# Optimization experiments

Measured on AMD Instinct MI355X. Metric: run time of the kernel, lower is better.

The kernel has to match this reference:

```python
import jax, jax.numpy as jnp
import numpy as np

D_MODEL = 512
N_HEADS = 8
HEAD_DIM = D_MODEL // N_HEADS
BATCH = 4
SEQ = 2048


def setup_inputs() -> dict:
    key = jax.random.key(0)
    ks = jax.random.split(key, 9)
    s = 1.0 / np.sqrt(D_MODEL)
    inp = {
        "x": jax.random.normal(ks[0], (BATCH, SEQ, D_MODEL), dtype=jnp.float32),
        "wq": jax.random.uniform(ks[1], (D_MODEL, D_MODEL), jnp.float32, -s, s),
        "bq": jax.random.uniform(ks[2], (D_MODEL,), jnp.float32, -s, s),
        "wk": jax.random.uniform(ks[3], (D_MODEL, D_MODEL), jnp.float32, -s, s),
        "bk": jax.random.uniform(ks[4], (D_MODEL,), jnp.float32, -s, s),
        "wv": jax.random.uniform(ks[5], (D_MODEL, D_MODEL), jnp.float32, -s, s),
        "bv": jax.random.uniform(ks[6], (D_MODEL,), jnp.float32, -s, s),
        "wo": jax.random.uniform(ks[7], (D_MODEL, D_MODEL), jnp.float32, -s, s),
        "bo": jax.random.uniform(ks[8], (D_MODEL,), jnp.float32, -s, s),
    }
    return inp


def reference(x, wq, bq, wk, bk, wv, bv, wo, bo):
    B, S, D = x.shape
    H, Hd = N_HEADS, HEAD_DIM
    # projections (torch Linear: y = x @ W^T + b; here weights stored as [in, out])
    q = (x @ wq + bq).reshape(B, S, H, Hd).transpose(0, 2, 1, 3)  # [B,H,S,Hd]
    k = (x @ wk + bk).reshape(B, S, H, Hd).transpose(0, 2, 1, 3)
    v = (x @ wv + bv).reshape(B, S, H, Hd).transpose(0, 2, 1, 3)
    scores = jnp.einsum("bhqd,bhkd->bhqk", q, k) / jnp.sqrt(jnp.float32(Hd))
    attn = jax.nn.softmax(scores, axis=-1)
    o = jnp.einsum("bhqk,bhkd->bhqd", attn, v)  # [B,H,S,Hd]
    o = o.transpose(0, 2, 1, 3).reshape(B, S, D)
    return o @ wo + bo
```

## Files before the change

kernel.cpp:

```cpp
#include <hip/hip_runtime.h>
#include <math.h>

#define DM   512
#define SEQL 2048
#define NB   4
#define NH   8
#define HD   64

typedef _Float16 f16;
typedef __fp16   fp16x2 __attribute__((ext_vector_type(2)));
typedef _Float16 f16x4 __attribute__((ext_vector_type(4)));
typedef _Float16 f16x8 __attribute__((ext_vector_type(8)));
typedef float    f32x4 __attribute__((ext_vector_type(4)));

#define QSCALE 0.1803368801f
#define SOFTMAX_SHIFT 4.328085123f
#define PSTR 88

typedef const __attribute__((address_space(1))) void* gp1_t;
typedef __attribute__((address_space(3))) void* lp3_t;
__device__ __forceinline__ void glds16(const void* g, void* l) {
    __builtin_amdgcn_global_load_lds((gp1_t)g, (lp3_t)l, 16, 0, 0);
}

__device__ __forceinline__ float fast_exp2(float x) {
    return __builtin_amdgcn_exp2f(x);
}

__global__ __launch_bounds__(256) void prep_kernel(
    const float* __restrict__ x, f16* __restrict__ xh,
    const float* __restrict__ w0, const float* __restrict__ w1,
    const float* __restrict__ w2, const float* __restrict__ w3,
    f16* __restrict__ o0, f16* __restrict__ o1,
    f16* __restrict__ o2, f16* __restrict__ o3)
{
    __shared__ f16 t[64][72];
    const int bx = blockIdx.x;
    if (bx < 2048) {
        int i = (bx * 256 + threadIdx.x) * 8;
        float4 a = *(const float4*)&x[i];
        float4 b = *(const float4*)&x[i + 4];
        f16x8 h;
        h[0] = (f16)a.x; h[1] = (f16)a.y; h[2] = (f16)a.z; h[3] = (f16)a.w;
        h[4] = (f16)b.x; h[5] = (f16)b.y; h[6] = (f16)b.z; h[7] = (f16)b.w;
        *(f16x8*)&xh[i] = h;
        return;
    }
    const int idx  = bx - 2048;
    const int wsel = idx >> 6, tile = idx & 63;
    const float* w; f16* o;
    switch (wsel) {
        case 0:  w = w0; o = o0; break;
        case 1:  w = w1; o = o1; break;
        case 2:  w = w2; o = o2; break;
        default: w = w3; o = o3; break;
    }
    const int n0 = (tile & 7) * 64, k0 = (tile >> 3) * 64;
    const int tx = threadIdx.x & 63, tg = threadIdx.x >> 6;
    #pragma unroll
    for (int r = 0; r < 16; ++r) {
        int kl = tg * 16 + r;
        t[tx][kl] = (f16)w[(size_t)(k0 + kl) * DM + n0 + tx];
    }
    __syncthreads();
    #pragma unroll
    for (int r = 0; r < 16; ++r) {
        int nl = tg * 16 + r;
        o[(size_t)(n0 + nl) * DM + k0 + tx] = t[nl][tx];
    }
}

__global__ __launch_bounds__(256) void gemm_qkv(
    const f16* __restrict__ A, const f16* __restrict__ Wt,
    const float* __restrict__ bq, const float* __restrict__ bk,
    const float* __restrict__ bv,
    f16* __restrict__ qh, f16* __restrict__ kh, f16* __restrict__ vth)
{
    __shared__ f16 As[2][128 * 32];
    __shared__ f16 Bs[2][128 * 32];

    const int tid  = threadIdx.x;
    const int lane = tid & 63, wave = tid >> 6;
    const int quad = lane >> 4, l15 = lane & 15;
    const int wm = wave >> 1, wn = wave & 1;

    const int bid = blockIdx.x;
    const int r8  = bid & 7;
    const int tt  = bid >> 3;
    const int j   = tt % 12;
    const int mm  = tt / 12;
    const int n0  = j * 128;
    const int m0  = (mm * 8 + r8) * 128;
    const bool qk = (j < 8);

    const int sr16 = lane >> 2;
    const int sk   = (lane & 3) * 8;

    f32x4 acc[4][4] = {};

    for (int k0 = 0; k0 < DM; k0 += 64) {
        #pragma unroll
        for (int kh2 = 0; kh2 < 2; ++kh2) {
            #pragma unroll
            for (int rb = 0; rb < 2; ++rb) {
                const int row = wave * 32 + rb * 16;
                glds16(&A [(size_t)(m0 + row + sr16) * DM + k0 + kh2 * 32 + sk],
                       &As[kh2][row * 32]);
                glds16(&Wt[(size_t)(n0 + row + sr16) * DM + k0 + kh2 * 32 + sk],
                       &Bs[kh2][row * 32]);
            }
        }
        __syncthreads();

        #pragma unroll
        for (int kh2 = 0; kh2 < 2; ++kh2) {
            f16x8 af[4], bf[4];
            #pragma unroll
            for (int i = 0; i < 4; ++i)
                af[i] = *(f16x8*)&As[kh2][(wm * 64 + i * 16 + l15) * 32 + quad * 8];
            #pragma unroll
            for (int i = 0; i < 4; ++i)
                bf[i] = *(f16x8*)&Bs[kh2][(wn * 64 + i * 16 + l15) * 32 + quad * 8];
            if (qk) {
                #pragma unroll
                for (int i = 0; i < 4; ++i)
                    #pragma unroll
                    for (int jj = 0; jj < 4; ++jj)
                        acc[i][jj] = __builtin_amdgcn_mfma_f32_16x16x32_f16(
                            bf[i], af[jj], acc[i][jj], 0, 0, 0);
            } else {
                #pragma unroll
                for (int i = 0; i < 4; ++i)
                    #pragma unroll
                    for (int jj = 0; jj < 4; ++jj)
                        acc[i][jj] = __builtin_amdgcn_mfma_f32_16x16x32_f16(
                            af[i], bf[jj], acc[i][jj], 0, 0, 0);
            }
        }
        __syncthreads();
    }

    const int nwave = n0 + wn * 64;
    const int seg   = nwave >> 9;
    const int nn0   = nwave & 511;
    const int h     = nn0 >> 6;

    if (qk) {
        f16* op = seg == 0 ? qh : kh;
        const float* bp = seg == 0 ? bq : bk;
        #pragma unroll
        for (int i = 0; i < 4; ++i) {
            const int hd = i * 16 + quad * 4;
            f32x4 bv4 = *(const f32x4*)&bp[nn0 + hd];
            #pragma unroll
            for (int jj = 0; jj < 4; ++jj) {
                const int m = m0 + wm * 64 + jj * 16 + l15;
                const int bb = m >> 11, s = m & 2047;
                f16x4 pk;
                #pragma unroll
                for (int rr = 0; rr < 4; ++rr) pk[rr] = (f16)(acc[i][jj][rr] + bv4[rr]);
                *(f16x4*)&op[(((size_t)(bb * NH + h) * SEQL + s) << 6) + hd] = pk;
            }
        }
    } else {
        #pragma unroll
        for (int jj = 0; jj < 4; ++jj) {
            const int hd = jj * 16 + l15;
            const float bias = bv[nn0 + hd];
            #pragma unroll
            for (int i = 0; i < 4; ++i) {
                const int mb = m0 + wm * 64 + i * 16 + quad * 4;
                const int bb = mb >> 11, s = mb & 2047;
                f16x4 pk;
                #pragma unroll
                for (int rr = 0; rr < 4; ++rr) pk[rr] = (f16)(acc[i][jj][rr] + bias);
                *(f16x4*)&vth[(((size_t)(bb * NH + h) * HD + hd) << 11) + s] = pk;
            }
        }
    }
}

__global__ __launch_bounds__(256) void gemm_out(
    const f16* __restrict__ A, const f16* __restrict__ Wt,
    const float* __restrict__ bias, float* __restrict__ out)
{
    __shared__ f16 As[2][64 * 32];
    __shared__ f16 Bs[2][128 * 32];

    const int tid  = threadIdx.x;
    const int lane = tid & 63, wave = tid >> 6;
    const int quad = lane >> 4, l15 = lane & 15;
    const int wn = wave >> 1, wm = wave & 1;
    const int n0 = blockIdx.x * 128, m0 = blockIdx.y * 64;

    const int sr16 = lane >> 2;
    const int sk   = (lane & 3) * 8;

    f32x4 acc[4][2] = {};

    for (int k0 = 0; k0 < DM; k0 += 64) {
        #pragma unroll
        for (int kh2 = 0; kh2 < 2; ++kh2) {
            {
                const int row = wave * 16;
                glds16(&A[(size_t)(m0 + row + sr16) * DM + k0 + kh2 * 32 + sk],
                       &As[kh2][row * 32]);
            }
            #pragma unroll
            for (int rb = 0; rb < 2; ++rb) {
                const int row = wave * 32 + rb * 16;
                glds16(&Wt[(size_t)(n0 + row + sr16) * DM + k0 + kh2 * 32 + sk],
                       &Bs[kh2][row * 32]);
            }
        }
        __syncthreads();

        #pragma unroll
        for (int kh2 = 0; kh2 < 2; ++kh2) {
            f16x8 af[4], bf[2];
            #pragma unroll
            for (int i = 0; i < 4; ++i)
                af[i] = *(f16x8*)&Bs[kh2][(wn * 64 + i * 16 + l15) * 32 + quad * 8];
            #pragma unroll
            for (int jj = 0; jj < 2; ++jj)
                bf[jj] = *(f16x8*)&As[kh2][(wm * 32 + jj * 16 + l15) * 32 + quad * 8];
            #pragma unroll
            for (int i = 0; i < 4; ++i)
                #pragma unroll
                for (int jj = 0; jj < 2; ++jj)
                    acc[i][jj] = __builtin_amdgcn_mfma_f32_16x16x32_f16(
                        af[i], bf[jj], acc[i][jj], 0, 0, 0);
        }
        __syncthreads();
    }

    #pragma unroll
    for (int i = 0; i < 4; ++i) {
        const int nb = n0 + wn * 64 + i * 16 + quad * 4;
        f32x4 bv4 = *(const f32x4*)&bias[nb];
        #pragma unroll
        for (int jj = 0; jj < 2; ++jj) {
            const int m = m0 + wm * 32 + jj * 16 + l15;
            f32x4 val = acc[i][jj] + bv4;
            *(f32x4*)&out[(size_t)m * DM + nb] = val;
        }
    }
}

__global__ __launch_bounds__(512) void flash_attn_mfma(
    const f16* __restrict__ Q, const f16* __restrict__ K,
    const f16* __restrict__ Vt, f16* __restrict__ O)
{
    __shared__ __align__(16) char smem[80896];
    f16*   Ks = (f16*)smem;
    f16*   Vs = (f16*)(smem + 18432);
    f16*   Ps = (f16*)(smem + 35840);
    float* cs = (float*)smem;
    float* Lx = (float*)(smem + 34816);

    const int tid  = threadIdx.x;
    const int lane = tid & 63, wave = tid >> 6;
    const int quad = lane >> 4, l15 = lane & 15;
    const int g  = wave >> 2;
    const int qg = wave & 3;

    const int id = blockIdx.x;
    const int r8 = id & 7;
    const int tt = id >> 3;
    const int j  = tt & 15;
    const int bh = (tt >> 4) * 8 + r8;
    const int q0 = j * 128;
    const int b = bh >> 3, h = bh & 7;
    f16* Pw = Ps + wave * (32 * PSTR);

    const f16* Qb = Q  + (size_t)bh * SEQL * HD;
    const f16* Kb = K  + (size_t)bh * SEQL * HD;
    const f16* Vb = Vt + (size_t)bh * HD * SEQL;

    f16x8 qf[2][2];
    #pragma unroll
    for (int mq = 0; mq < 2; ++mq)
        #pragma unroll
        for (int ks = 0; ks < 2; ++ks) {
            qf[mq][ks] = *(const f16x8*)
                &Qb[(size_t)(q0 + qg * 32 + mq * 16 + l15) * HD + ks * 32 + quad * 8];
            #pragma unroll
            for (int jj = 0; jj < 8; ++jj) qf[mq][ks][jj] *= (f16)QSCALE;
        }

    f16x8 onesf;
    #pragma unroll
    for (int jj = 0; jj < 8; ++jj) onesf[jj] = (f16)1.0f;

    const int krow = tid >> 3, kch = (tid & 7) * 8;
    const int vrow = tid >> 4, vch = (tid & 15) * 8;

    f16x8 kreg[2], vreg[2];
    #pragma unroll
    for (int r = 0; r < 2; ++r) {
        kreg[r] = *(const f16x8*)&Kb[(size_t)(krow + r * 64) * HD + kch];
        vreg[r] = *(const f16x8*)&Vb[(size_t)(vrow + r * 32) * SEQL + vch];
    }

    f32x4 o_acc[2][4] = {};
    f32x4 o_l[2] = {};

    for (int kt = 0; kt < SEQL / 128; ++kt) {
        __syncthreads();
        #pragma unroll
        for (int r = 0; r < 2; ++r) {
            *(f16x8*)&Ks[(krow + r * 64) * 72 + kch]  = kreg[r];
            *(f16x8*)&Vs[(vrow + r * 32) * 136 + vch] = vreg[r];
        }
        __syncthreads();
        if (kt < SEQL / 128 - 1) {
            const int kb2 = (kt + 1) * 128;
            #pragma unroll
            for (int r = 0; r < 2; ++r) {
                kreg[r] = *(const f16x8*)&Kb[(size_t)(kb2 + krow + r * 64) * HD + kch];
                vreg[r] = *(const f16x8*)&Vb[(size_t)(vrow + r * 32) * SEQL + kb2 + vch];
            }
        }

        f32x4 sc[4][2];
        #pragma unroll
        for (int mk = 0; mk < 4; ++mk)
            #pragma unroll
            for (int mq = 0; mq < 2; ++mq)
                sc[mk][mq] = (f32x4){-SOFTMAX_SHIFT, -SOFTMAX_SHIFT,
                                     -SOFTMAX_SHIFT, -SOFTMAX_SHIFT};
        #pragma unroll
        for (int ks = 0; ks < 2; ++ks) {
            #pragma unroll
            for (int mk = 0; mk < 4; ++mk) {
                f16x8 af = *(f16x8*)&Ks[(g * 64 + mk * 16 + l15) * 72 + ks * 32 + quad * 8];
                #pragma unroll
                for (int mq = 0; mq < 2; ++mq)
                    sc[mk][mq] = __builtin_amdgcn_mfma_f32_16x16x32_f16(
                        af, qf[mq][ks], sc[mk][mq], 0, 0, 0);
            }
        }

        #pragma unroll
        for (int mk = 0; mk < 4; ++mk)
            #pragma unroll
            for (int mq = 0; mq < 2; ++mq) {
                float p0 = fast_exp2(sc[mk][mq][0]);
                float p1 = fast_exp2(sc[mk][mq][1]);
                float p2 = fast_exp2(sc[mk][mq][2]);
                float p3 = fast_exp2(sc[mk][mq][3]);
                union { f16x4 v4; fp16x2 v2[2]; } pk;
                pk.v2[0] = __builtin_amdgcn_cvt_pkrtz(p0, p1);
                pk.v2[1] = __builtin_amdgcn_cvt_pkrtz(p2, p3);
                *(f16x4*)&Pw[(mq * 16 + l15) * PSTR + mk * 16 + quad * 4] = pk.v4;
            }

        #pragma unroll
        for (int kc = 0; kc < 2; ++kc) {
            f16x8 pa0 = *(f16x8*)&Pw[(l15)      * PSTR + kc * 32 + quad * 8];
            f16x8 pa1 = *(f16x8*)&Pw[(16 + l15) * PSTR + kc * 32 + quad * 8];
            o_l[0] = __builtin_amdgcn_mfma_f32_16x16x32_f16(pa0, onesf, o_l[0], 0, 0, 0);
            o_l[1] = __builtin_amdgcn_mfma_f32_16x16x32_f16(pa1, onesf, o_l[1], 0, 0, 0);
            #pragma unroll
            for (int nt = 0; nt < 4; ++nt) {
                f16x8 vb = *(f16x8*)&Vs[(nt * 16 + l15) * 136 + g * 64 + kc * 32 + quad * 8];
                o_acc[0][nt] = __builtin_amdgcn_mfma_f32_16x16x32_f16(
                    pa0, vb, o_acc[0][nt], 0, 0, 0);
                o_acc[1][nt] = __builtin_amdgcn_mfma_f32_16x16x32_f16(
                    pa1, vb, o_acc[1][nt], 0, 0, 0);
            }
        }
    }

    __syncthreads();
    if (l15 == 0) {
        #pragma unroll
        for (int mq = 0; mq < 2; ++mq)
            #pragma unroll
            for (int r = 0; r < 4; ++r)
                Lx[wave * 32 + mq * 16 + quad * 4 + r] = o_l[mq][r];
    }
    if (g == 1) {
        #pragma unroll
        for (int mq = 0; mq < 2; ++mq)
            #pragma unroll
            for (int r = 0; r < 4; ++r) {
                const int ql = mq * 16 + quad * 4 + r;
                #pragma unroll
                for (int nt = 0; nt < 4; ++nt)
                    cs[(qg * 32 + ql) * 68 + nt * 16 + l15] = o_acc[mq][nt][r];
            }
    }
    __syncthreads();
    if (g == 0) {
        #pragma unroll
        for (int mq = 0; mq < 2; ++mq)
            #pragma unroll
            for (int r = 0; r < 4; ++r) {
                const int ql = mq * 16 + quad * 4 + r;
                const float inv = 1.0f / (Lx[qg * 32 + ql] + Lx[(4 + qg) * 32 + ql]);
                const int s = q0 + qg * 32 + ql;
                #pragma unroll
                for (int nt = 0; nt < 4; ++nt) {
                    float ov = o_acc[mq][nt][r] + cs[(qg * 32 + ql) * 68 + nt * 16 + l15];
                    O[((size_t)(b * SEQL + s)) * DM + h * HD + nt * 16 + l15] =
                        (f16)(ov * inv);
                }
            }
    }
}

extern "C" void kernel_launch(void* const* d_in, const int* in_sizes, int n_in,
                              void* d_out, int out_size, void* d_ws, size_t ws_size,
                              hipStream_t stream) {
    const float* x  = (const float*)d_in[0];
    const float* wq = (const float*)d_in[1];
    const float* bq = (const float*)d_in[2];
    const float* wk = (const float*)d_in[3];
    const float* bk = (const float*)d_in[4];
    const float* wv = (const float*)d_in[5];
    const float* bv = (const float*)d_in[6];
    const float* wo = (const float*)d_in[7];
    const float* bo = (const float*)d_in[8];

    const size_t NE = (size_t)NB * SEQL * DM;
    const size_t WE = (size_t)DM * DM;
    f16* xh    = (f16*)d_ws;
    f16* wqkvt = xh + NE;
    f16* wot   = wqkvt + 3 * WE;
    f16* qh    = wot + WE;
    f16* kh    = qh + NE;
    f16* vth   = kh + NE;
    f16* oh    = vth + NE;

    prep_kernel<<<2304, 256, 0, stream>>>(
        x, xh, wq, wk, wv, wo,
        wqkvt, wqkvt + WE, wqkvt + 2 * WE, wot);

    gemm_qkv<<<768, 256, 0, stream>>>(
        xh, wqkvt, bq, bk, bv, qh, kh, vth);

    flash_attn_mfma<<<512, 512, 0, stream>>>(qh, kh, vth, oh);

    gemm_out<<<dim3(4, 128), 256, 0, stream>>>(oh, wot, bo, (float*)d_out);
}
```

Baseline: 175.7 us.

## Load V fragments directly from global into registers, dropping V LDS staging

Removes the shared-memory staging of the transposed V tile. Each wave now loads its V MFMA operands straight from global memory, in two halves issued around the QK^T MFMAs. This cuts LDS stores and reads and shrinks the shared allocation, which could allow more blocks per CU. In exchange, the four query-group waves sharing a key half each fetch the same V data from global/L2, and the loads sit on the critical path within the iteration instead of being prefetched one tile ahead.

```diff
diff --git a/kernel.cpp b/kernel.cpp
--- a/kernel.cpp
+++ b/kernel.cpp
@@ -251,10 +251,9 @@
     const f16* __restrict__ Q, const f16* __restrict__ K,
     const f16* __restrict__ Vt, f16* __restrict__ O)
 {
-    __shared__ __align__(16) char smem[80896];
+    __shared__ __align__(16) char smem[63488];
     f16*   Ks = (f16*)smem;
-    f16*   Vs = (f16*)(smem + 18432);
-    f16*   Ps = (f16*)(smem + 35840);
+    f16*   Ps = (f16*)(smem + 18432);
     float* cs = (float*)smem;
     float* Lx = (float*)(smem + 34816);
 
@@ -293,14 +292,11 @@
     for (int jj = 0; jj < 8; ++jj) onesf[jj] = (f16)1.0f;
 
     const int krow = tid >> 3, kch = (tid & 7) * 8;
-    const int vrow = tid >> 4, vch = (tid & 15) * 8;
-
-    f16x8 kreg[2], vreg[2];
-    #pragma unroll
-    for (int r = 0; r < 2; ++r) {
+
+    f16x8 kreg[2];
+    #pragma unroll
+    for (int r = 0; r < 2; ++r)
         kreg[r] = *(const f16x8*)&Kb[(size_t)(krow + r * 64) * HD + kch];
-        vreg[r] = *(const f16x8*)&Vb[(size_t)(vrow + r * 32) * SEQL + vch];
-    }
 
     f32x4 o_acc[2][4] = {};
     f32x4 o_l[2] = {};
@@ -308,19 +304,23 @@
     for (int kt = 0; kt < SEQL / 128; ++kt) {
         __syncthreads();
         #pragma unroll
-        for (int r = 0; r < 2; ++r) {
-            *(f16x8*)&Ks[(krow + r * 64) * 72 + kch]  = kreg[r];
-            *(f16x8*)&Vs[(vrow + r * 32) * 136 + vch] = vreg[r];
-        }
+        for (int r = 0; r < 2; ++r)
+            *(f16x8*)&Ks[(krow + r * 64) * 72 + kch] = kreg[r];
         __syncthreads();
         if (kt < SEQL / 128 - 1) {
             const int kb2 = (kt + 1) * 128;
             #pragma unroll
-            for (int r = 0; r < 2; ++r) {
+            for (int r = 0; r < 2; ++r)
                 kreg[r] = *(const f16x8*)&Kb[(size_t)(kb2 + krow + r * 64) * HD + kch];
-                vreg[r] = *(const f16x8*)&Vb[(size_t)(vrow + r * 32) * SEQL + kb2 + vch];
-            }
-        }
+        }
+
+        const int kgl = kt * 128 + g * 64;
+
+        f16x8 vf[2][4];
+        #pragma unroll
+        for (int nt = 0; nt < 4; ++nt)
+            vf[0][nt] = *(const f16x8*)
+                &Vb[(size_t)(nt * 16 + l15) * SEQL + kgl + quad * 8];
 
         f32x4 sc[4][2];
         #pragma unroll
@@ -340,6 +340,11 @@
                         af, qf[mq][ks], sc[mk][mq], 0, 0, 0);
             }
         }
+
+        #pragma unroll
+        for (int nt = 0; nt < 4; ++nt)
+            vf[1][nt] = *(const f16x8*)
+                &Vb[(size_t)(nt * 16 + l15) * SEQL + kgl + 32 + quad * 8];
 
         #pragma unroll
         for (int mk = 0; mk < 4; ++mk)
@@ -363,11 +368,10 @@
             o_l[1] = __builtin_amdgcn_mfma_f32_16x16x32_f16(pa1, onesf, o_l[1], 0, 0, 0);
             #pragma unroll
             for (int nt = 0; nt < 4; ++nt) {
-                f16x8 vb = *(f16x8*)&Vs[(nt * 16 + l15) * 136 + g * 64 + kc * 32 + quad * 8];
                 o_acc[0][nt] = __builtin_amdgcn_mfma_f32_16x16x32_f16(
-                    pa0, vb, o_acc[0][nt], 0, 0, 0);
+                    pa0, vf[kc][nt], o_acc[0][nt], 0, 0, 0);
                 o_acc[1][nt] = __builtin_amdgcn_mfma_f32_16x16x32_f16(
-                    pa1, vb, o_acc[1][nt], 0, 0, 0);
+                    pa1, vf[kc][nt], o_acc[1][nt], 0, 0, 0);
             }
         }
     }
```

After: 215.8 us. 1.23x slower.
